# Kernel optimization log

Hardware: AMD Instinct MI355X
Metric: run time of the kernel (lower is better)

Reference implementation:

```python
import jax, jax.numpy as jnp
import numpy as np

B, L, D = 256, 200, 512


def setup_inputs() -> dict:
    key = jax.random.key(0)
    ks = jax.random.split(key, 13)
    s = 0.04  # ~1/sqrt(D) init scale
    return {
        "session_emb": jax.random.normal(ks[0], (B, L, D), jnp.float32),
        "target_emb": jax.random.normal(ks[1], (B, D), jnp.float32),
        # attention projection (torch.rand in original; scaled for stable softmax)
        "w": jax.random.uniform(ks[2], (D, D), jnp.float32) * s,
        # nn.GRU params (PyTorch layout: weight_ih_l0 [3D, D] in r,z,n order)
        "gru_wih": jax.random.normal(ks[3], (3 * D, D), jnp.float32) * s,
        "gru_whh": jax.random.normal(ks[4], (3 * D, D), jnp.float32) * s,
        "gru_bih": jax.random.normal(ks[5], (3 * D,), jnp.float32) * s,
        "gru_bhh": jax.random.normal(ks[6], (3 * D,), jnp.float32) * s,
        # AUGRUCell: three Linear(2D -> D); input is cat([h_prev, x])
        "reset_w": jax.random.normal(ks[7], (D, 2 * D), jnp.float32) * s,
        "reset_b": jax.random.normal(ks[8], (D,), jnp.float32) * s,
        "update_w": jax.random.normal(ks[9], (D, 2 * D), jnp.float32) * s,
        "update_b": jax.random.normal(ks[10], (D,), jnp.float32) * s,
        "hhat_w": jax.random.normal(ks[11], (D, 2 * D), jnp.float32) * s,
        "hhat_b": jax.random.normal(ks[12], (D,), jnp.float32) * s,
    }


def reference(session_emb, target_emb, w, gru_wih, gru_whh, gru_bih, gru_bhh,
              reset_w, reset_b, update_w, update_b, hhat_w, hhat_b):
    b, l, d = session_emb.shape
    # --- nn.GRU (1 layer, batch_first, h0 = 0). Precompute input projections.
    x_proj = jnp.einsum('bld,ed->ble', session_emb, gru_wih) + gru_bih  # [B,L,3D]

    def gru_step(h, xp):
        hp = h @ gru_whh.T + gru_bhh  # [B,3D]
        xr, xz, xn = jnp.split(xp, 3, axis=-1)
        hr, hz, hn = jnp.split(hp, 3, axis=-1)
        r = jax.nn.sigmoid(xr + hr)
        z = jax.nn.sigmoid(xz + hz)
        n = jnp.tanh(xn + r * hn)
        h_new = (1.0 - z) * n + z * h
        return h_new, h_new

    h0 = jnp.zeros((b, d), session_emb.dtype)
    h_last, s_seq = jax.lax.scan(gru_step, h0, jnp.swapaxes(x_proj, 0, 1))  # s_seq [L,B,D]
    s_state = jnp.swapaxes(s_seq, 0, 1)  # [B,L,D]

    # --- attention = softmax_over_seq( (s_state @ w) @ target ) -> [B,L,1]
    logits = jnp.einsum('bld,de,be->bl', s_state, w, target_emb)
    att = jax.nn.softmax(logits, axis=1)[..., None]  # [B,L,1]

    # --- AUGRU over timesteps, init h = GRU final hidden state
    def augru_step(h, inp):
        x, a = inp  # x: [B,D], a: [B,1]
        ti = jnp.concatenate([h, x], axis=-1)  # cat([h_prev, x])
        r = jax.nn.sigmoid(ti @ reset_w.T + reset_b)
        u = jax.nn.sigmoid(ti @ update_w.T + update_b)
        hh = jnp.tanh(jnp.concatenate([h * r, x], axis=-1) @ hhat_w.T + hhat_b)
        u = a * u
        h_new = (1.0 - u) * h + u * hh
        return h_new, None

    h_final, _ = jax.lax.scan(augru_step, h_last, (s_seq, jnp.swapaxes(att, 0, 1)))
    return h_final
```

## Files before the change

kernel.cpp:

```cpp
#include <hip/hip_runtime.h>
#include <math.h>

#define NL 200
#define SLICE 131072ul

#define BIG_OFF   0ul
#define LG_OFF    26345472ul
#define ATT_OFF   26396672ul
#define VT_OFF    26447872ul
#define HBUF_OFF  26578944ul
#define HR_OFF    26841088ul
#define FLAGS_OFF 26972160ul
#define HAUG_OFF  26973184ul
#define HRAUG_OFF (HAUG_OFF + 200ul * SLICE)
#define WS_NEED_FLOATS (HRAUG_OFF + 200ul * SLICE)

typedef __attribute__((ext_vector_type(2))) __fp16 h2;

__device__ __forceinline__ float sigmoidf_(float x) { return 1.0f / (1.0f + expf(-x)); }

__device__ __forceinline__ unsigned pk2(float a, float b) {
  union { h2 h; unsigned u; } x;
  x.h.x = (__fp16)a; x.h.y = (__fp16)b;
  return x.u;
}
__device__ __forceinline__ h2 pkh(float a, float b) {
  h2 r; r.x = (__fp16)a; r.y = (__fp16)b; return r;
}
__device__ __forceinline__ float fd2(unsigned w, h2 a, float c) {
  union { unsigned u; h2 h; } x; x.u = w;
  return __builtin_amdgcn_fdot2(a, x.h, c, false);
}

__device__ __forceinline__ float cohld1(const float* p) {
  return __hip_atomic_load(p, __ATOMIC_RELAXED, __HIP_MEMORY_SCOPE_AGENT);
}
__device__ __forceinline__ float2 cohld2(const float* p) {
  union { double d; float2 f; } u;
  u.d = __hip_atomic_load((const double*)p, __ATOMIC_RELAXED, __HIP_MEMORY_SCOPE_AGENT);
  return u.f;
}
__device__ __forceinline__ void cohst1(float* p, float v) {
  __hip_atomic_store(p, v, __ATOMIC_RELAXED, __HIP_MEMORY_SCOPE_AGENT);
}

__device__ __forceinline__ void gwait64(const unsigned* f, unsigned val) {
  const int i = threadIdx.x & 63;
  int guard = 0;
  while (__hip_atomic_load(f + i, __ATOMIC_RELAXED, __HIP_MEMORY_SCOPE_AGENT) < val) {
    if (++guard > (1 << 22)) break;
  }
}
__device__ __forceinline__ void gwait128(const unsigned* f, unsigned val) {
  const int i = threadIdx.x & 63;
  bool d0 = false, d1 = false;
  int guard = 0;
  while (!(d0 && d1)) {
    if (!d0) d0 = __hip_atomic_load(f + i, __ATOMIC_RELAXED, __HIP_MEMORY_SCOPE_AGENT) >= val;
    if (!d1) d1 = __hip_atomic_load(f + i + 64, __ATOMIC_RELAXED, __HIP_MEMORY_SCOPE_AGENT) >= val;
    if (++guard > (1 << 22)) break;
  }
}

__global__ void init_kernel(float* __restrict__ ws) {
  unsigned* const fl = (unsigned*)(ws + FLAGS_OFF);
  for (int j = threadIdx.x; j < 768; j += 256) fl[j] = 0u;
}

__global__ __launch_bounds__(256) void transpose_kernel(const float* __restrict__ in,
                                                        float* __restrict__ ws) {
  __shared__ float tile[64][65];
  const int tx = threadIdx.x & 63, ty = threadIdx.x >> 6;
  const size_t tk0 = (size_t)blockIdx.x * 64;
  const int b0 = blockIdx.y * 64;
#pragma unroll
  for (int r = 0; r < 16; ++r) {
    const int bb = ty + 4 * r;
    tile[bb][tx] = in[(size_t)(b0 + bb) * 102400 + tk0 + tx];
  }
  __syncthreads();
  float* const big1 = ws + BIG_OFF + SLICE;
#pragma unroll
  for (int r = 0; r < 16; ++r) {
    const int kk = ty + 4 * r;
    cohst1(big1 + (tk0 + kk) * 256 + b0 + tx, tile[tx][kk]);
  }
}

__global__ __launch_bounds__(256) void vt_kernel(const float* __restrict__ w,
                                                 const float* __restrict__ tgt,
                                                 float* __restrict__ ws) {
  __shared__ float t_s[512];
  const int b = blockIdx.x, tid = threadIdx.x;
  for (int i = tid; i < 512; i += 256) t_s[i] = tgt[(size_t)b * 512 + i];
  __syncthreads();
  const int wv = tid >> 6, lane = tid & 63;
  for (int d = wv; d < 512; d += 4) {
    const float* const wr = w + (size_t)d * 512;
    const float4 a  = *(const float4*)(wr + lane * 8);
    const float4 a2 = *(const float4*)(wr + lane * 8 + 4);
    float s = a.x * t_s[lane * 8 + 0] + a.y * t_s[lane * 8 + 1] +
              a.z * t_s[lane * 8 + 2] + a.w * t_s[lane * 8 + 3] +
              a2.x * t_s[lane * 8 + 4] + a2.y * t_s[lane * 8 + 5] +
              a2.z * t_s[lane * 8 + 6] + a2.w * t_s[lane * 8 + 7];
    for (int off = 32; off > 0; off >>= 1) s += __shfl_xor(s, off);
    if (lane == 0) ws[VT_OFF + (size_t)d * 256 + b] = s;
  }
}

__global__ __launch_bounds__(512) void gru_kernel(const float* __restrict__ wih,
                                                  const float* __restrict__ whh,
                                                  const float* __restrict__ bih,
                                                  const float* __restrict__ bhh,
                                                  float* __restrict__ ws) {
  __shared__ float wxT[512 * 16];
  __shared__ float whT[512 * 16];
  __shared__ float red[16 * 8 * 130];
  __shared__ float bihs[12], bhhs[12];

  const int bg = blockIdx.x >> 7;
  const int ng = blockIdx.x & 127;
  const int b0 = bg << 7, c0 = ng << 2;
  const int tid = threadIdx.x;

  for (int i = tid; i < 512 * 16; i += 512) {
    const int k = i >> 4, s = i & 15;
    if (s < 12) {
      const int grow = ((s >> 2) << 9) + c0 + (s & 3);
      wxT[i] = wih[(size_t)grow * 512 + k];
      whT[i] = whh[(size_t)grow * 512 + k];
    }
  }
  if (tid < 12) {
    const int grow = ((tid >> 2) << 9) + c0 + (tid & 3);
    bihs[tid] = bih[grow];
    bhhs[tid] = bhh[grow];
  }
  __syncthreads();

  float* const big = ws + BIG_OFF;
  unsigned* const gf = (unsigned*)(ws + FLAGS_OFF) + (bg << 7);

  const int wv = tid >> 6, l = tid & 63;
  const int k0 = wv << 6;
  const int boff = b0 + 2 * l;
  const int qg = tid >> 7;
  const int rr = tid & 127;
  const size_t og = (size_t)(c0 + qg) * 256 + b0 + rr;

  float2 ax[12];
#pragma unroll
  for (int s = 0; s < 12; ++s) ax[s] = make_float2(0.0f, 0.0f);
  {
    const float* const xp = big + 1ul * SLICE + boff;
    for (int bq = 0; bq < 4; ++bq) {
      const int kb = k0 + bq * 16;
      float2 v[16];
#pragma unroll
      for (int j = 0; j < 16; ++j) v[j] = cohld2(xp + (size_t)(kb + j) * 256);
#pragma unroll
      for (int j = 0; j < 16; ++j) {
        const float4* const wr = (const float4*)(wxT + (size_t)(kb + j) * 16);
        float w12[12];
        *(float4*)&w12[0] = wr[0];
        *(float4*)&w12[4] = wr[1];
        *(float4*)&w12[8] = wr[2];
#pragma unroll
        for (int s = 0; s < 12; ++s) {
          ax[s].x += v[j].x * w12[s];
          ax[s].y += v[j].y * w12[s];
        }
      }
    }
  }

  for (int t = 0; t < NL; ++t) {
    if (t > 0) {
      if (wv == 0) gwait128(gf, (unsigned)t);
      __syncthreads();
    }
    float2 ah[12];
#pragma unroll
    for (int s = 0; s < 12; ++s) ah[s] = make_float2(0.0f, 0.0f);
    float hprev = 0.0f;
    if (t > 0) {
      const float* const hp = big + (size_t)(t - 1) * SLICE + boff;
      hprev = big[(size_t)(t - 1) * SLICE + og];
      for (int bq = 0; bq < 4; ++bq) {
        const int kb = k0 + bq * 16;
        float2 v[16];
#pragma unroll
        for (int j = 0; j < 16; ++j) v[j] = *(const float2*)(hp + (size_t)(kb + j) * 256);
#pragma unroll
        for (int j = 0; j < 16; ++j) {
          const float4* const wr = (const float4*)(whT + (size_t)(kb + j) * 16);
          float w12[12];
          *(float4*)&w12[0] = wr[0];
          *(float4*)&w12[4] = wr[1];
          *(float4*)&w12[8] = wr[2];
#pragma unroll
          for (int s = 0; s < 12; ++s) {
            ah[s].x += v[j].x * w12[s];
            ah[s].y += v[j].y * w12[s];
          }
        }
      }
    }
#pragma unroll
    for (int s = 0; s < 4; ++s) {
      *(float2*)&red[((size_t)(0 + s) * 8 + wv) * 130 + 2 * l] =
          make_float2(ax[s].x + ah[s].x, ax[s].y + ah[s].y);
      *(float2*)&red[((size_t)(4 + s) * 8 + wv) * 130 + 2 * l] =
          make_float2(ax[4 + s].x + ah[4 + s].x, ax[4 + s].y + ah[4 + s].y);
      *(float2*)&red[((size_t)(8 + s) * 8 + wv) * 130 + 2 * l] = ax[8 + s];
      *(float2*)&red[((size_t)(12 + s) * 8 + wv) * 130 + 2 * l] = ah[8 + s];
    }
    __syncthreads();
    float rp = 0, zp = 0, xnp = 0, hnp = 0;
#pragma unroll
    for (int w8 = 0; w8 < 8; ++w8) {
      rp  += red[((size_t)(0 + qg) * 8 + w8) * 130 + rr];
      zp  += red[((size_t)(4 + qg) * 8 + w8) * 130 + rr];
      xnp += red[((size_t)(8 + qg) * 8 + w8) * 130 + rr];
      hnp += red[((size_t)(12 + qg) * 8 + w8) * 130 + rr];
    }
    const float r = sigmoidf_(rp + bihs[0 + qg] + bhhs[0 + qg]);
    const float z = sigmoidf_(zp + bihs[4 + qg] + bhhs[4 + qg]);
    const float n = tanhf(xnp + bihs[8 + qg] + r * (hnp + bhhs[8 + qg]));
    const float hnew = (1.0f - z) * n + z * hprev;
    cohst1(big + (size_t)t * SLICE + og, hnew);
    asm volatile("s_waitcnt vmcnt(0)" ::: "memory");
    __syncthreads();
    if (tid == 0)
      __hip_atomic_store(gf + ng, (unsigned)(t + 1), __ATOMIC_RELAXED, __HIP_MEMORY_SCOPE_AGENT);
    if (t + 1 < NL) {
      const float* const xp = big + (size_t)(t + 2) * SLICE + boff;
#pragma unroll
      for (int s = 0; s < 12; ++s) ax[s] = make_float2(0.0f, 0.0f);
      for (int bq = 0; bq < 4; ++bq) {
        const int kb = k0 + bq * 16;
        float2 v[16];
#pragma unroll
        for (int j = 0; j < 16; ++j) v[j] = cohld2(xp + (size_t)(kb + j) * 256);
#pragma unroll
        for (int j = 0; j < 16; ++j) {
          const float4* const wr = (const float4*)(wxT + (size_t)(kb + j) * 16);
          float w12[12];
          *(float4*)&w12[0] = wr[0];
          *(float4*)&w12[4] = wr[1];
          *(float4*)&w12[8] = wr[2];
#pragma unroll
          for (int s = 0; s < 12; ++s) {
            ax[s].x += v[j].x * w12[s];
            ax[s].y += v[j].y * w12[s];
          }
        }
      }
    }
    asm volatile("" ::: "memory");
  }
}

__global__ __launch_bounds__(256) void attn1_kernel(float* __restrict__ ws) {
  const int l = blockIdx.x, tid = threadIdx.x;
  const float* const sl = ws + BIG_OFF + (size_t)l * SLICE + tid;
  const float* const vtt = ws + VT_OFF + tid;
  float acc = 0.0f;
#pragma unroll 8
  for (int k = 0; k < 512; ++k)
    acc += sl[(size_t)k * 256] * vtt[(size_t)k * 256];
  ws[LG_OFF + (size_t)l * 256 + tid] = acc;
}

__global__ __launch_bounds__(256) void attn2_kernel(float* __restrict__ ws) {
  __shared__ float red[8];
  const int b = blockIdx.x, tid = threadIdx.x;
  const float v = (tid < NL) ? ws[LG_OFF + (size_t)tid * 256 + b] : -3.0e38f;
  float m = v;
  for (int off = 32; off > 0; off >>= 1) m = fmaxf(m, __shfl_xor(m, off));
  if ((tid & 63) == 0) red[tid >> 6] = m;
  __syncthreads();
  m = fmaxf(fmaxf(red[0], red[1]), fmaxf(red[2], red[3]));
  const float e = (tid < NL) ? expf(v - m) : 0.0f;
  float s = e;
  for (int off = 32; off > 0; off >>= 1) s += __shfl_xor(s, off);
  __syncthreads();
  if ((tid & 63) == 0) red[4 + (tid >> 6)] = s;
  __syncthreads();
  s = red[4] + red[5] + red[6] + red[7];
  if (tid < NL) ws[ATT_OFF + (size_t)tid * 256 + b] = e / s;
}

template <bool COH, int NQ, int SOFF, int WOFF>
__device__ __forceinline__ void adot(const float* ap, const unsigned* wT24,
                                     int kp0, float* acc) {
  for (int g = 0; g < 4; ++g) {
    const int kb = kp0 + g * 8;
    float va[8], vb[8];
#pragma unroll
    for (int j = 0; j < 8; ++j) {
      const float* p0 = ap + (size_t)(2 * (kb + j)) * 256;
      if (COH) { va[j] = cohld1(p0); vb[j] = cohld1(p0 + 256); }
      else     { va[j] = p0[0]; vb[j] = p0[256]; }
    }
#pragma unroll
    for (int j = 0; j < 8; ++j) {
      const h2 r = pkh(va[j], vb[j]);
      const uint4* wq = (const uint4*)(wT24 + (size_t)(WOFF + kb + j) * 24) + SOFF;
#pragma unroll
      for (int q = 0; q < NQ; ++q) {
        const uint4 qq = wq[q];
        acc[4 * q + 0] = fd2(qq.x, r, acc[4 * q + 0]);
        acc[4 * q + 1] = fd2(qq.y, r, acc[4 * q + 1]);
        acc[4 * q + 2] = fd2(qq.z, r, acc[4 * q + 2]);
        acc[4 * q + 3] = fd2(qq.w, r, acc[4 * q + 3]);
      }
    }
  }
}

template <bool EXP>
__global__ __launch_bounds__(512) void augru_kernel(const float* __restrict__ rw,
                                                    const float* __restrict__ rbias,
                                                    const float* __restrict__ uw,
                                                    const float* __restrict__ ubias,
                                                    const float* __restrict__ hw,
                                                    const float* __restrict__ hbias,
                                                    float* __restrict__ ws,
                                                    float* __restrict__ out) {
  __shared__ unsigned wT[512 * 24];
  __shared__ float red[24 * 8 * 66];
  __shared__ float rbs[8], ubs[8], hbs[8];

  const int rg = blockIdx.x >> 6;
  const int cg = blockIdx.x & 63;
  const int r0 = rg << 6, c0 = cg << 3;
  const int tid = threadIdx.x;

  for (int i = tid; i < 512 * 24; i += 512) {
    const int kp = i / 24, s = i % 24;
    const int m = s >> 3, c = s & 7;
    const float* const wm = (m == 0) ? rw : (m == 1) ? uw : hw;
    wT[i] = pk2(wm[(size_t)(c0 + c) * 1024 + 2 * kp],
                wm[(size_t)(c0 + c) * 1024 + 2 * kp + 1]);
  }
  if (tid < 8) {
    rbs[tid] = rbias[c0 + tid];
    ubs[tid] = ubias[c0 + tid];
    hbs[tid] = hbias[c0 + tid];
  }
  __syncthreads();

  float* const big = ws + BIG_OFF;
  float* const hbuf = ws + HBUF_OFF;
  float* const hrg = ws + HR_OFF;
  float* const haug = ws + HAUG_OFF;
  float* const hraug = ws + HRAUG_OFF;
  const float* const att = ws + ATT_OFF;
  unsigned* const fbase = (unsigned*)(ws + FLAGS_OFF);
  unsigned* const af1 = fbase + 256 + (rg << 6);
  unsigned* const af2 = fbase + 512 + (rg << 6);

  const int wv = tid >> 6, l = tid & 63;
  const int kp0 = wv << 5;
  const int boff = r0 + l;
  const int cq = tid >> 6;
  const int rr = tid & 63;
  const size_t og = (size_t)(c0 + cq) * 256 + r0 + rr;

  float ax[24];
#pragma unroll
  for (int s = 0; s < 24; ++s) ax[s] = 0.0f;
  adot<false, 6, 0, 256>(big + boff, wT, kp0, ax);

  for (int t = 0; t < NL; ++t) {
    if (t > 0) {
      if (wv == 0) gwait64(af2, (unsigned)t);
      __syncthreads();
    }
    const float* const hsrc =
        (t == 0) ? (big + 199ul * SLICE)
                 : (EXP ? (haug + (size_t)(t - 1) * SLICE)
                        : (hbuf + (size_t)(t & 1) * SLICE));
    float hcur;
    if (EXP) hcur = hsrc[og]; else hcur = cohld1(hsrc + og);
    float ah[16];
#pragma unroll
    for (int s = 0; s < 16; ++s) ah[s] = 0.0f;
    if (EXP) adot<false, 4, 0, 0>(hsrc + boff, wT, kp0, ah);
    else     adot<true, 4, 0, 0>(hsrc + boff, wT, kp0, ah);
#pragma unroll
    for (int c = 0; c < 8; ++c) {
      red[((size_t)(0 + c) * 8 + wv) * 66 + l] = ax[c] + ah[c];
      red[((size_t)(8 + c) * 8 + wv) * 66 + l] = ax[8 + c] + ah[8 + c];
      red[((size_t)(16 + c) * 8 + wv) * 66 + l] = ax[16 + c];
    }
    __syncthreads();
    float rp = 0, up = 0, xhp = 0;
#pragma unroll
    for (int w8 = 0; w8 < 8; ++w8) {
      rp  += red[((size_t)(0 + cq) * 8 + w8) * 66 + rr];
      up  += red[((size_t)(8 + cq) * 8 + w8) * 66 + rr];
      xhp += red[((size_t)(16 + cq) * 8 + w8) * 66 + rr];
    }
    const float rgate = sigmoidf_(rp + rbs[cq]);
    const float ug = sigmoidf_(up + ubs[cq]);
    float* const hrdst = EXP ? (hraug + (size_t)t * SLICE) : hrg;
    cohst1(hrdst + og, rgate * hcur);
    asm volatile("s_waitcnt vmcnt(0)" ::: "memory");
    __syncthreads();
    if (tid == 0)
      __hip_atomic_store(af1 + cg, (unsigned)(t + 1), __ATOMIC_RELAXED, __HIP_MEMORY_SCOPE_AGENT);
    if (t + 1 < NL) {
#pragma unroll
      for (int s = 0; s < 24; ++s) ax[s] = 0.0f;
      adot<false, 6, 0, 256>(big + (size_t)(t + 1) * SLICE + boff, wT, kp0, ax);
    }
    asm volatile("" ::: "memory");
    if (wv == 0) gwait64(af1, (unsigned)(t + 1));
    __syncthreads();
    float ahh[8];
#pragma unroll
    for (int s = 0; s < 8; ++s) ahh[s] = 0.0f;
    {
      const float* const rp2 = (EXP ? (hraug + (size_t)t * SLICE) : hrg) + boff;
      if (EXP) adot<false, 2, 4, 0>(rp2, wT, kp0, ahh);
      else     adot<true, 2, 4, 0>(rp2, wT, kp0, ahh);
    }
#pragma unroll
    for (int c = 0; c < 8; ++c)
      red[((size_t)c * 8 + wv) * 66 + l] = ahh[c];
    __syncthreads();
    float hhp = 0;
#pragma unroll
    for (int w8 = 0; w8 < 8; ++w8)
      hhp += red[((size_t)cq * 8 + w8) * 66 + rr];
    const float hh = tanhf(hhp + xhp + hbs[cq]);
    const float av = att[(size_t)t * 256 + r0 + rr];
    const float u = av * ug;
    const float hn = (1.0f - u) * hcur + u * hh;
    if (t == NL - 1) {
      out[(size_t)(r0 + rr) * 512 + c0 + cq] = hn;
    } else {
      float* const hdst = EXP ? (haug + (size_t)t * SLICE)
                              : (hbuf + (size_t)((t + 1) & 1) * SLICE);
      cohst1(hdst + og, hn);
    }
    asm volatile("s_waitcnt vmcnt(0)" ::: "memory");
    __syncthreads();
    if (tid == 0)
      __hip_atomic_store(af2 + cg, (unsigned)(t + 1), __ATOMIC_RELAXED, __HIP_MEMORY_SCOPE_AGENT);
  }
}

extern "C" void kernel_launch(void* const* d_in, const int* in_sizes, int n_in,
                              void* d_out, int out_size, void* d_ws, size_t ws_size,
                              hipStream_t stream) {
  (void)in_sizes; (void)n_in; (void)out_size;
  const float* session = (const float*)d_in[0];
  const float* target  = (const float*)d_in[1];
  const float* w       = (const float*)d_in[2];
  const float* wih     = (const float*)d_in[3];
  const float* whh     = (const float*)d_in[4];
  const float* bih     = (const float*)d_in[5];
  const float* bhh     = (const float*)d_in[6];
  const float* rw      = (const float*)d_in[7];
  const float* rb      = (const float*)d_in[8];
  const float* uw      = (const float*)d_in[9];
  const float* ub      = (const float*)d_in[10];
  const float* hw      = (const float*)d_in[11];
  const float* hb      = (const float*)d_in[12];
  float* ws  = (float*)d_ws;
  float* out = (float*)d_out;

  const bool expanded = ws_size >= WS_NEED_FLOATS * 4ul;

  hipLaunchKernelGGL(init_kernel, dim3(1), dim3(256), 0, stream, ws);
  hipLaunchKernelGGL(transpose_kernel, dim3(1600, 4), dim3(256), 0, stream, session, ws);
  hipLaunchKernelGGL(vt_kernel, dim3(256), dim3(256), 0, stream, w, target, ws);
  hipLaunchKernelGGL(gru_kernel, dim3(256), dim3(512), 0, stream,
                     wih, whh, bih, bhh, ws);
  hipLaunchKernelGGL(attn1_kernel, dim3(200), dim3(256), 0, stream, ws);
  hipLaunchKernelGGL(attn2_kernel, dim3(256), dim3(256), 0, stream, ws);
  if (expanded) {
    hipLaunchKernelGGL(augru_kernel<true>, dim3(256), dim3(512), 0, stream,
                       rw, rb, uw, ub, hw, hb, ws, out);
  } else {
    hipLaunchKernelGGL(augru_kernel<false>, dim3(256), dim3(512), 0, stream,
                       rw, rb, uw, ub, hw, hb, ws, out);
  }
}
```

Measured before the change: 7.135 ms.

## Store AUGRU hidden states in place over consumed GRU slices in workspace

Removes the two code paths (expanded separate haug/hraug buffers vs double-buffered hbuf) and writes each AUGRU hidden state into the workspace slice of the GRU sequence that was just consumed, so reads of h use plain loads from a single-writer location. The x-projection reads of the GRU states switch to coherent loads because those slices are now overwritten by other blocks, and the hhat dot uses a deeper load batch (16). This cuts workspace footprint and keeps a fresh, uncached address per step, at the cost of more coherent loads on the input projection.

Measured after the change: 7.245 ms. Within noise of the previous version (+1.5%).

```diff
diff --git a/kernel.cpp b/kernel.cpp
--- a/kernel.cpp
+++ b/kernel.cpp
@@ -8,12 +8,8 @@
 #define LG_OFF    26345472ul
 #define ATT_OFF   26396672ul
 #define VT_OFF    26447872ul
-#define HBUF_OFF  26578944ul
 #define HR_OFF    26841088ul
 #define FLAGS_OFF 26972160ul
-#define HAUG_OFF  26973184ul
-#define HRAUG_OFF (HAUG_OFF + 200ul * SLICE)
-#define WS_NEED_FLOATS (HRAUG_OFF + 200ul * SLICE)
 
 typedef __attribute__((ext_vector_type(2))) __fp16 h2;
 
@@ -291,20 +287,20 @@
   if (tid < NL) ws[ATT_OFF + (size_t)tid * 256 + b] = e / s;
 }
 
-template <bool COH, int NQ, int SOFF, int WOFF>
+template <bool COH, int NQ, int SOFF, int WOFF, int DEPTH>
 __device__ __forceinline__ void adot(const float* ap, const unsigned* wT24,
                                      int kp0, float* acc) {
-  for (int g = 0; g < 4; ++g) {
-    const int kb = kp0 + g * 8;
-    float va[8], vb[8];
-#pragma unroll
-    for (int j = 0; j < 8; ++j) {
+  for (int g = 0; g < 32 / DEPTH; ++g) {
+    const int kb = kp0 + g * DEPTH;
+    float va[DEPTH], vb[DEPTH];
+#pragma unroll
+    for (int j = 0; j < DEPTH; ++j) {
       const float* p0 = ap + (size_t)(2 * (kb + j)) * 256;
       if (COH) { va[j] = cohld1(p0); vb[j] = cohld1(p0 + 256); }
       else     { va[j] = p0[0]; vb[j] = p0[256]; }
     }
 #pragma unroll
-    for (int j = 0; j < 8; ++j) {
+    for (int j = 0; j < DEPTH; ++j) {
       const h2 r = pkh(va[j], vb[j]);
       const uint4* wq = (const uint4*)(wT24 + (size_t)(WOFF + kb + j) * 24) + SOFF;
 #pragma unroll
@@ -319,7 +315,6 @@
   }
 }
 
-template <bool EXP>
 __global__ __launch_bounds__(512) void augru_kernel(const float* __restrict__ rw,
                                                     const float* __restrict__ rbias,
                                                     const float* __restrict__ uw,
@@ -352,10 +347,7 @@
   __syncthreads();
 
   float* const big = ws + BIG_OFF;
-  float* const hbuf = ws + HBUF_OFF;
   float* const hrg = ws + HR_OFF;
-  float* const haug = ws + HAUG_OFF;
-  float* const hraug = ws + HRAUG_OFF;
   const float* const att = ws + ATT_OFF;
   unsigned* const fbase = (unsigned*)(ws + FLAGS_OFF);
   unsigned* const af1 = fbase + 256 + (rg << 6);
@@ -371,7 +363,7 @@
   float ax[24];
 #pragma unroll
   for (int s = 0; s < 24; ++s) ax[s] = 0.0f;
-  adot<false, 6, 0, 256>(big + boff, wT, kp0, ax);
+  adot<true, 6, 0, 256, 8>(big + boff, wT, kp0, ax);
 
   for (int t = 0; t < NL; ++t) {
     if (t > 0) {
@@ -379,16 +371,12 @@
       __syncthreads();
     }
     const float* const hsrc =
-        (t == 0) ? (big + 199ul * SLICE)
-                 : (EXP ? (haug + (size_t)(t - 1) * SLICE)
-                        : (hbuf + (size_t)(t & 1) * SLICE));
-    float hcur;
-    if (EXP) hcur = hsrc[og]; else hcur = cohld1(hsrc + og);
+        big + ((t == 0) ? 199ul : (t == 1) ? 200ul : (size_t)(t - 1)) * SLICE;
+    const float hcur = hsrc[og];
     float ah[16];
 #pragma unroll
     for (int s = 0; s < 16; ++s) ah[s] = 0.0f;
-    if (EXP) adot<false, 4, 0, 0>(hsrc + boff, wT, kp0, ah);
-    else     adot<true, 4, 0, 0>(hsrc + boff, wT, kp0, ah);
+    adot<false, 4, 0, 0, 8>(hsrc + boff, wT, kp0, ah);
 #pragma unroll
     for (int c = 0; c < 8; ++c) {
       red[((size_t)(0 + c) * 8 + wv) * 66 + l] = ax[c] + ah[c];
@@ -405,8 +393,7 @@
     }
     const float rgate = sigmoidf_(rp + rbs[cq]);
     const float ug = sigmoidf_(up + ubs[cq]);
-    float* const hrdst = EXP ? (hraug + (size_t)t * SLICE) : hrg;
-    cohst1(hrdst + og, rgate * hcur);
+    cohst1(hrg + og, rgate * hcur);
     asm volatile("s_waitcnt vmcnt(0)" ::: "memory");
     __syncthreads();
     if (tid == 0)
@@ -414,7 +401,7 @@
     if (t + 1 < NL) {
 #pragma unroll
       for (int s = 0; s < 24; ++s) ax[s] = 0.0f;
-      adot<false, 6, 0, 256>(big + (size_t)(t + 1) * SLICE + boff, wT, kp0, ax);
+      adot<true, 6, 0, 256, 8>(big + (size_t)(t + 1) * SLICE + boff, wT, kp0, ax);
     }
     asm volatile("" ::: "memory");
     if (wv == 0) gwait64(af1, (unsigned)(t + 1));
@@ -422,11 +409,7 @@
     float ahh[8];
 #pragma unroll
     for (int s = 0; s < 8; ++s) ahh[s] = 0.0f;
-    {
-      const float* const rp2 = (EXP ? (hraug + (size_t)t * SLICE) : hrg) + boff;
-      if (EXP) adot<false, 2, 4, 0>(rp2, wT, kp0, ahh);
-      else     adot<true, 2, 4, 0>(rp2, wT, kp0, ahh);
-    }
+    adot<true, 2, 4, 0, 16>(hrg + boff, wT, kp0, ahh);
 #pragma unroll
     for (int c = 0; c < 8; ++c)
       red[((size_t)c * 8 + wv) * 66 + l] = ahh[c];
@@ -442,8 +425,7 @@
     if (t == NL - 1) {
       out[(size_t)(r0 + rr) * 512 + c0 + cq] = hn;
     } else {
-      float* const hdst = EXP ? (haug + (size_t)t * SLICE)
-                              : (hbuf + (size_t)((t + 1) & 1) * SLICE);
+      float* const hdst = big + ((t == 0) ? 200ul : (size_t)t) * SLICE;
       cohst1(hdst + og, hn);
     }
     asm volatile("s_waitcnt vmcnt(0)" ::: "memory");
@@ -456,7 +438,7 @@
 extern "C" void kernel_launch(void* const* d_in, const int* in_sizes, int n_in,
                               void* d_out, int out_size, void* d_ws, size_t ws_size,
                               hipStream_t stream) {
-  (void)in_sizes; (void)n_in; (void)out_size;
+  (void)in_sizes; (void)n_in; (void)out_size; (void)ws_size;
   const float* session = (const float*)d_in[0];
   const float* target  = (const float*)d_in[1];
   const float* w       = (const float*)d_in[2];
@@ -473,8 +455,6 @@
   float* ws  = (float*)d_ws;
   float* out = (float*)d_out;
 
-  const bool expanded = ws_size >= WS_NEED_FLOATS * 4ul;
-
   hipLaunchKernelGGL(init_kernel, dim3(1), dim3(256), 0, stream, ws);
   hipLaunchKernelGGL(transpose_kernel, dim3(1600, 4), dim3(256), 0, stream, session, ws);
   hipLaunchKernelGGL(vt_kernel, dim3(256), dim3(256), 0, stream, w, target, ws);
@@ -482,11 +462,6 @@
                      wih, whh, bih, bhh, ws);
   hipLaunchKernelGGL(attn1_kernel, dim3(200), dim3(256), 0, stream, ws);
   hipLaunchKernelGGL(attn2_kernel, dim3(256), dim3(256), 0, stream, ws);
-  if (expanded) {
-    hipLaunchKernelGGL(augru_kernel<true>, dim3(256), dim3(512), 0, stream,
-                       rw, rb, uw, ub, hw, hb, ws, out);
-  } else {
-    hipLaunchKernelGGL(augru_kernel<false>, dim3(256), dim3(512), 0, stream,
-                       rw, rb, uw, ub, hw, hb, ws, out);
-  }
-}
+  hipLaunchKernelGGL(augru_kernel, dim3(256), dim3(512), 0, stream,
+                     rw, rb, uw, ub, hw, hb, ws, out);
+}
```
